# Performance work log

Measured on AMD Instinct MI355X. Metric: run time of the kernel, lower is better.

Reference implementation:

```python
import jax, jax.numpy as jnp
import numpy as np

B, N, DIN, DH, DOUT, E = 262144, 8, 3, 32, 1, 32


def setup_inputs() -> dict:
    key = jax.random.key(0)
    ks = jax.random.split(key, 8)
    x = jax.random.normal(ks[0], (B, N, DIN), dtype=jnp.float32)
    edge_index = jax.random.randint(ks[1], (2, E), 0, N, dtype=jnp.int64)
    s = lambda k, sh: jax.random.normal(k, sh, dtype=jnp.float32) * 0.1
    return {
        "x": x,
        "edge_index": edge_index,
        "W1": s(ks[2], (DIN, DH)),
        "b1": jnp.zeros((DH,), jnp.float32),
        "W2": s(ks[3], (DH, DH)),
        "b2": jnp.zeros((DH,), jnp.float32),
        "Wout": s(ks[4], (DH, DOUT)),
        "bout": jnp.zeros((DOUT,), jnp.float32),
    }


def _gcn_norm(edge_index, n):
    # add self loops, symmetric GCN normalization D^-1/2 (A+I) D^-1/2
    loops = jnp.arange(n, dtype=edge_index.dtype)
    src = jnp.concatenate([edge_index[0], loops])
    dst = jnp.concatenate([edge_index[1], loops])
    deg = jnp.zeros((n,), jnp.float32).at[dst].add(1.0)
    dinv = jax.lax.rsqrt(jnp.maximum(deg, 1e-12))
    norm = dinv[src] * dinv[dst]  # [E+N]
    return src, dst, norm


def _gcn_layer(h, W, b, src, dst, norm):
    hw = h @ W                              # [B, N, H]
    msg = hw[:, src, :] * norm[None, :, None]
    agg = jnp.zeros_like(hw).at[:, dst, :].add(msg)
    return agg + b


def reference(x, edge_index, W1, b1, W2, b2, Wout, bout):
    n = x.shape[1]
    src, dst, norm = _gcn_norm(edge_index, n)
    h = jax.nn.relu(_gcn_layer(x, W1, b1, src, dst, norm))
    h = jax.nn.relu(_gcn_layer(h, W2, b2, src, dst, norm))
    h = jax.nn.relu(h @ Wout + bout)        # [B, N, DOUT]
    # global_mean_pool with all-zero batch ids == mean over nodes
    return jnp.mean(h, axis=1)              # [B, DOUT]
```

## Files before the change

### kernel.cpp

```cpp
#include <hip/hip_runtime.h>


typedef __bf16 bf16x8 __attribute__((ext_vector_type(8)));
typedef float  f32x16 __attribute__((ext_vector_type(16)));

#define GPT 32
#define TPB 8

__global__ __launch_bounds__(256, 2) void gnn_kernel(
    const float* __restrict__ x,
    const int* __restrict__ ei,
    const float* __restrict__ W1,
    const float* __restrict__ b1,
    const float* __restrict__ W2,
    const float* __restrict__ b2,
    const float* __restrict__ Wout,
    const float* __restrict__ bout,
    float* __restrict__ out,
    int B)
{
    __shared__ float As[64];
    __shared__ float degs[8], dinvs[8];
    __shared__ float W1s[96], b1s[32], W2s[1024], b2s[32], Wouts[32];
    __shared__ float xs[TPB * GPT * 24];

    const int tid = threadIdx.x;

    if (tid < 96) W1s[tid] = W1[tid];
    if (tid < 64) As[tid] = 0.0f;
    if (tid < 32) { b1s[tid] = b1[tid]; b2s[tid] = b2[tid]; Wouts[tid] = Wout[tid]; }
    if (tid < 8)  degs[tid] = 1.0f;
    for (int i = tid; i < 1024; i += 256) W2s[i] = W2[i];
    {
        const float4* x4 = reinterpret_cast<const float4*>(x);
        long long base4 = (long long)blockIdx.x * (TPB * GPT * 6);
        float4* xs4 = reinterpret_cast<float4*>(xs);
        #pragma unroll
        for (int i = 0; i < 6; i++)
            xs4[tid + 256 * i] = x4[base4 + tid + 256 * i];
    }
    __syncthreads();
    if (tid < 32) { int d = ei[32 + tid]; atomicAdd(&degs[d], 1.0f); }
    __syncthreads();
    if (tid < 8) dinvs[tid] = 1.0f / sqrtf(degs[tid]);
    __syncthreads();
    if (tid < 32) {
        int s = ei[tid], d = ei[32 + tid];
        atomicAdd(&As[d * 8 + s], dinvs[s] * dinvs[d]);
    } else if (tid < 40) {
        int n = tid - 32;
        atomicAdd(&As[n * 8 + n], dinvs[n] * dinvs[n]);
    }
    __syncthreads();

    const int lane = tid & 63;
    const int wv   = tid >> 6;
    const int r    = lane & 31;
    const int q    = lane >> 5;
    const int n8   = r & 7;
    const int gl   = r >> 3;
    const int g0   = wv * 4 + gl;
    const int g1   = 16 + wv * 4 + gl;

    float arow[8];
    #pragma unroll
    for (int m = 0; m < 8; m++) arow[m] = As[n8 * 8 + m];

    bf16x8 w1Ahi, w1Alo;
    #pragma unroll
    for (int j = 0; j < 8; j++) { w1Ahi[j] = (__bf16)0.0f; w1Alo[j] = (__bf16)0.0f; }
    #pragma unroll
    for (int j = 0; j < 3; j++) {
        float v = W1s[j * 32 + r];
        __bf16 h = (__bf16)v;
        w1Ahi[j] = h; w1Alo[j] = (__bf16)(v - (float)h);
    }
    {
        float v = b1s[r];
        __bf16 h = (__bf16)v;
        w1Ahi[3] = h; w1Alo[3] = (__bf16)(v - (float)h);
    }

    bf16x8 w2hi[2];
    #pragma unroll
    for (int s = 0; s < 2; s++) {
        #pragma unroll
        for (int j = 0; j < 8; j++) {
            int kk = 8 * s + j;
            int hid = (kk & 3) + 8 * (kk >> 2) + 4 * q;
            w2hi[s][j] = (__bf16)W2s[hid * 32 + r];
        }
    }
    bf16x8 a32hi[2];
    #pragma unroll
    for (int s = 0; s < 2; s++) {
        #pragma unroll
        for (int j = 0; j < 8; j++) {
            int kk = 8 * s + j;
            float v = ((kk >> 2) == gl) ? arow[(kk & 3) + 4 * q] : 0.0f;
            a32hi[s][j] = (__bf16)v;
        }
    }
    f32x16 zerov, b2rv;
    float woutr[16];
    #pragma unroll
    for (int k = 0; k < 16; k++) {
        int hk = (k & 3) + 8 * (k >> 2) + 4 * q;
        zerov[k] = 0.0f;
        b2rv[k] = b2s[hk];
        woutr[k] = Wouts[hk];
    }
    const float boutv = bout[0];

    #pragma unroll 4
    for (int it = 0; it < TPB; it++) {
        const long long gbase = ((long long)blockIdx.x * TPB + it) * GPT;
        const float* xt = &xs[it * GPT * 24];

        float y00 = 0.f, y01 = 0.f, y02 = 0.f;
        {
            float xv[24];
            #pragma unroll
            for (int i = 0; i < 6; i++) {
                float4 v = *reinterpret_cast<const float4*>(&xt[g0 * 24 + i * 4]);
                xv[4 * i] = v.x; xv[4 * i + 1] = v.y; xv[4 * i + 2] = v.z; xv[4 * i + 3] = v.w;
            }
            #pragma unroll
            for (int m = 0; m < 8; m++) {
                y00 = fmaf(arow[m], xv[m * 3 + 0], y00);
                y01 = fmaf(arow[m], xv[m * 3 + 1], y01);
                y02 = fmaf(arow[m], xv[m * 3 + 2], y02);
            }
        }
        float y10 = 0.f, y11 = 0.f, y12 = 0.f;
        {
            float xv[24];
            #pragma unroll
            for (int i = 0; i < 6; i++) {
                float4 v = *reinterpret_cast<const float4*>(&xt[g1 * 24 + i * 4]);
                xv[4 * i] = v.x; xv[4 * i + 1] = v.y; xv[4 * i + 2] = v.z; xv[4 * i + 3] = v.w;
            }
            #pragma unroll
            for (int m = 0; m < 8; m++) {
                y10 = fmaf(arow[m], xv[m * 3 + 0], y10);
                y11 = fmaf(arow[m], xv[m * 3 + 1], y11);
                y12 = fmaf(arow[m], xv[m * 3 + 2], y12);
            }
        }

        bf16x8 yB0, yB1;
        #pragma unroll
        for (int j = 0; j < 8; j++) { yB0[j] = (__bf16)0.0f; yB1[j] = (__bf16)0.0f; }
        {
            __bf16 h0 = (__bf16)y00, h1 = (__bf16)y01, h2 = (__bf16)y02;
            yB0[0] = q ? (__bf16)(y00 - (float)h0) : h0;
            yB0[1] = q ? (__bf16)(y01 - (float)h1) : h1;
            yB0[2] = q ? (__bf16)(y02 - (float)h2) : h2;
            yB0[3] = q ? (__bf16)0.0f : (__bf16)1.0f;
            __bf16 g0h = (__bf16)y10, g1h = (__bf16)y11, g2h = (__bf16)y12;
            yB1[0] = q ? (__bf16)(y10 - (float)g0h) : g0h;
            yB1[1] = q ? (__bf16)(y11 - (float)g1h) : g1h;
            yB1[2] = q ? (__bf16)(y12 - (float)g2h) : g2h;
            yB1[3] = q ? (__bf16)0.0f : (__bf16)1.0f;
        }

        f32x16 vacc0, vacc1;
        vacc0 = __builtin_amdgcn_mfma_f32_32x32x16_bf16(w1Ahi, yB0, zerov, 0, 0, 0);
        vacc1 = __builtin_amdgcn_mfma_f32_32x32x16_bf16(w1Ahi, yB1, zerov, 0, 0, 0);
        vacc0 = __builtin_amdgcn_mfma_f32_32x32x16_bf16(w1Alo, yB0, vacc0, 0, 0, 0);
        vacc1 = __builtin_amdgcn_mfma_f32_32x32x16_bf16(w1Alo, yB1, vacc1, 0, 0, 0);

        bf16x8 phi0[2], phi1[2];
        #pragma unroll
        for (int s = 0; s < 2; s++) {
            #pragma unroll
            for (int j = 0; j < 8; j++) {
                phi0[s][j] = (__bf16)fmaxf(vacc0[8 * s + j], 0.0f);
                phi1[s][j] = (__bf16)fmaxf(vacc1[8 * s + j], 0.0f);
            }
        }

        vacc0 = __builtin_amdgcn_mfma_f32_32x32x16_bf16(phi0[0], w2hi[0], zerov, 0, 0, 0);
        vacc1 = __builtin_amdgcn_mfma_f32_32x32x16_bf16(phi1[0], w2hi[0], zerov, 0, 0, 0);
        vacc0 = __builtin_amdgcn_mfma_f32_32x32x16_bf16(phi0[1], w2hi[1], vacc0, 0, 0, 0);
        vacc1 = __builtin_amdgcn_mfma_f32_32x32x16_bf16(phi1[1], w2hi[1], vacc1, 0, 0, 0);

        bf16x8 thi0[2], thi1[2];
        #pragma unroll
        for (int s = 0; s < 2; s++) {
            #pragma unroll
            for (int j = 0; j < 8; j++) {
                thi0[s][j] = (__bf16)vacc0[8 * s + j];
                thi1[s][j] = (__bf16)vacc1[8 * s + j];
            }
        }

        vacc0 = __builtin_amdgcn_mfma_f32_32x32x16_bf16(thi0[0], a32hi[0], b2rv, 0, 0, 0);
        vacc1 = __builtin_amdgcn_mfma_f32_32x32x16_bf16(thi1[0], a32hi[0], b2rv, 0, 0, 0);
        vacc0 = __builtin_amdgcn_mfma_f32_32x32x16_bf16(thi0[1], a32hi[1], vacc0, 0, 0, 0);
        vacc1 = __builtin_amdgcn_mfma_f32_32x32x16_bf16(thi1[1], a32hi[1], vacc1, 0, 0, 0);

        float ss0 = 0.0f, ss1 = 0.0f;
        #pragma unroll
        for (int k = 0; k < 16; k++) {
            ss0 = fmaf(fmaxf(vacc0[k], 0.0f), woutr[k], ss0);
            ss1 = fmaf(fmaxf(vacc1[k], 0.0f), woutr[k], ss1);
        }
        ss0 += __shfl_xor(ss0, 32, 64);
        ss1 += __shfl_xor(ss1, 32, 64);
        float o0 = fmaxf(ss0 + boutv, 0.0f);
        float o1 = fmaxf(ss1 + boutv, 0.0f);
        o0 += __shfl_xor(o0, 1, 64);  o1 += __shfl_xor(o1, 1, 64);
        o0 += __shfl_xor(o0, 2, 64);  o1 += __shfl_xor(o1, 2, 64);
        o0 += __shfl_xor(o0, 4, 64);  o1 += __shfl_xor(o1, 4, 64);
        if (q == 0 && n8 == 0) {
            long long gg0 = gbase + g0;
            if (gg0 < (long long)B) out[gg0] = o0 * 0.125f;
            long long gg1 = gbase + g1;
            if (gg1 < (long long)B) out[gg1] = o1 * 0.125f;
        }
    }
}

extern "C" void kernel_launch(void* const* d_in, const int* in_sizes, int n_in,
                              void* d_out, int out_size, void* d_ws, size_t ws_size,
                              hipStream_t stream) {
    const float* x    = (const float*)d_in[0];
    const int*   ei   = (const int*)d_in[1];
    const float* W1   = (const float*)d_in[2];
    const float* b1   = (const float*)d_in[3];
    const float* W2   = (const float*)d_in[4];
    const float* b2   = (const float*)d_in[5];
    const float* Wout = (const float*)d_in[6];
    const float* bout = (const float*)d_in[7];
    float* out = (float*)d_out;
    (void)d_ws; (void)ws_size; (void)out_size; (void)n_in;

    const int B = in_sizes[0] / 24;
    const int grid = B / (TPB * GPT);
    gnn_kernel<<<grid, 256, 0, stream>>>(x, ei, W1, b1, W2, b2, Wout, bout, out, B);
}
```

Baseline: 30.64 us.

## Pack hi/lo split terms into one MFMA K dimension and double tiles per block

```diff
diff --git a/kernel.cpp b/kernel.cpp
--- a/kernel.cpp
+++ b/kernel.cpp
@@ -5,7 +5,7 @@
 typedef float  f32x16 __attribute__((ext_vector_type(16)));
 
 #define GPT 32
-#define TPB 8
+#define TPB 16
 
 __global__ __launch_bounds__(256, 2) void gnn_kernel(
     const float* __restrict__ x,
@@ -36,7 +36,7 @@
         long long base4 = (long long)blockIdx.x * (TPB * GPT * 6);
         float4* xs4 = reinterpret_cast<float4*>(xs);
         #pragma unroll
-        for (int i = 0; i < 6; i++)
+        for (int i = 0; i < 12; i++)
             xs4[tid + 256 * i] = x4[base4 + tid + 256 * i];
     }
     __syncthreads();
@@ -66,19 +66,26 @@
     #pragma unroll
     for (int m = 0; m < 8; m++) arow[m] = As[n8 * 8 + m];
 
-    bf16x8 w1Ahi, w1Alo;
-    #pragma unroll
-    for (int j = 0; j < 8; j++) { w1Ahi[j] = (__bf16)0.0f; w1Alo[j] = (__bf16)0.0f; }
-    #pragma unroll
-    for (int j = 0; j < 3; j++) {
-        float v = W1s[j * 32 + r];
-        __bf16 h = (__bf16)v;
-        w1Ahi[j] = h; w1Alo[j] = (__bf16)(v - (float)h);
-    }
+    bf16x8 w1A;
     {
-        float v = b1s[r];
-        __bf16 h = (__bf16)v;
-        w1Ahi[3] = h; w1Alo[3] = (__bf16)(v - (float)h);
+        __bf16 h[3], l[3];
+        #pragma unroll
+        for (int j = 0; j < 3; j++) {
+            float v = W1s[j * 32 + r];
+            h[j] = (__bf16)v;
+            l[j] = (__bf16)(v - (float)h[j]);
+        }
+        float bv = b1s[r];
+        __bf16 bh = (__bf16)bv;
+        __bf16 bl = (__bf16)(bv - (float)bh);
+        w1A[0] = q ? l[0] : h[0];
+        w1A[1] = q ? l[1] : h[1];
+        w1A[2] = q ? l[2] : h[2];
+        w1A[3] = q ? l[0] : bh;
+        w1A[4] = q ? l[1] : h[0];
+        w1A[5] = q ? l[2] : h[1];
+        w1A[6] = q ? (__bf16)0.0f : h[2];
+        w1A[7] = q ? (__bf16)0.0f : bl;
     }
 
     bf16x8 w2hi[2];
@@ -149,26 +156,32 @@
         }
 
         bf16x8 yB0, yB1;
-        #pragma unroll
-        for (int j = 0; j < 8; j++) { yB0[j] = (__bf16)0.0f; yB1[j] = (__bf16)0.0f; }
         {
             __bf16 h0 = (__bf16)y00, h1 = (__bf16)y01, h2 = (__bf16)y02;
-            yB0[0] = q ? (__bf16)(y00 - (float)h0) : h0;
-            yB0[1] = q ? (__bf16)(y01 - (float)h1) : h1;
-            yB0[2] = q ? (__bf16)(y02 - (float)h2) : h2;
-            yB0[3] = q ? (__bf16)0.0f : (__bf16)1.0f;
-            __bf16 g0h = (__bf16)y10, g1h = (__bf16)y11, g2h = (__bf16)y12;
-            yB1[0] = q ? (__bf16)(y10 - (float)g0h) : g0h;
-            yB1[1] = q ? (__bf16)(y11 - (float)g1h) : g1h;
-            yB1[2] = q ? (__bf16)(y12 - (float)g2h) : g2h;
-            yB1[3] = q ? (__bf16)0.0f : (__bf16)1.0f;
+            __bf16 l0 = (__bf16)(y00 - (float)h0);
+            __bf16 l1 = (__bf16)(y01 - (float)h1);
+            __bf16 l2 = (__bf16)(y02 - (float)h2);
+            yB0[0] = h0; yB0[1] = h1; yB0[2] = h2;
+            yB0[3] = q ? l0 : (__bf16)1.0f;
+            yB0[4] = q ? l1 : l0;
+            yB0[5] = q ? l2 : l1;
+            yB0[6] = q ? (__bf16)0.0f : l2;
+            yB0[7] = q ? (__bf16)0.0f : (__bf16)1.0f;
+            __bf16 m0 = (__bf16)y10, m1 = (__bf16)y11, m2 = (__bf16)y12;
+            __bf16 n0 = (__bf16)(y10 - (float)m0);
+            __bf16 n1 = (__bf16)(y11 - (float)m1);
+            __bf16 n2 = (__bf16)(y12 - (float)m2);
+            yB1[0] = m0; yB1[1] = m1; yB1[2] = m2;
+            yB1[3] = q ? n0 : (__bf16)1.0f;
+            yB1[4] = q ? n1 : n0;
+            yB1[5] = q ? n2 : n1;
+            yB1[6] = q ? (__bf16)0.0f : n2;
+            yB1[7] = q ? (__bf16)0.0f : (__bf16)1.0f;
         }
 
         f32x16 vacc0, vacc1;
-        vacc0 = __builtin_amdgcn_mfma_f32_32x32x16_bf16(w1Ahi, yB0, zerov, 0, 0, 0);
-        vacc1 = __builtin_amdgcn_mfma_f32_32x32x16_bf16(w1Ahi, yB1, zerov, 0, 0, 0);
-        vacc0 = __builtin_amdgcn_mfma_f32_32x32x16_bf16(w1Alo, yB0, vacc0, 0, 0, 0);
-        vacc1 = __builtin_amdgcn_mfma_f32_32x32x16_bf16(w1Alo, yB1, vacc1, 0, 0, 0);
+        vacc0 = __builtin_amdgcn_mfma_f32_32x32x16_bf16(w1A, yB0, zerov, 0, 0, 0);
+        vacc1 = __builtin_amdgcn_mfma_f32_32x32x16_bf16(w1A, yB1, zerov, 0, 0, 0);
 
         bf16x8 phi0[2], phi1[2];
         #pragma unroll
```

Measured after the change: 31.04 us. No clear change (+1.3%).
